# Optimization experiments

Measured on AMD Instinct MI355X. Metric: run time of the kernel, lower is better.

The kernel has to match this reference:

```python
import jax, jax.numpy as jnp
import numpy as np

N_NODES = 100000
N_EDGES = 3200000
DIM = 16


def setup_inputs() -> dict:
    key = jax.random.key(0)
    k1, k2, k3, k4 = jax.random.split(key, 4)
    state_input = jax.random.normal(k1, (N_NODES, DIM), dtype=jnp.float32)
    row = jax.random.randint(k2, (N_EDGES,), 0, N_NODES, dtype=jnp.int32)
    col = jax.random.randint(k3, (N_EDGES,), 0, N_NODES, dtype=jnp.int32)
    edge_weights = jax.random.uniform(k4, (N_EDGES,), dtype=jnp.float32)
    return {"state_input": state_input, "row": row, "col": col,
            "edge_weights": edge_weights}


def reference(state_input, row, col, edge_weights):
    # f_eq: per-dim self dynamics, f(x) = -x  -> [N, dim]
    self_diff = -state_input

    # gather pair endpoints: x_1 = state[col], x_2 = state[row]
    # g_eq: sin(x_2 - x_1) per dim (Kuramoto-style coupling) -> [E, dim]
    neighbor_processed = jnp.sin(state_input[row] - state_input[col])

    # weight by edge weight and scatter-sum into destination nodes (col)
    aggregated_sum = jax.ops.segment_sum(
        neighbor_processed * edge_weights[:, None], col,
        num_segments=state_input.shape[0])  # [N, dim]

    # s_eq: elementwise tanh on aggregated sum
    interact_diff = jnp.tanh(aggregated_sum)

    return (self_diff + interact_diff,
            (state_input, self_diff),
            (aggregated_sum, interact_diff))
```

## Files before the change

kernel.cpp:

```cpp
#include <hip/hip_runtime.h>
#include <hip/hip_fp16.h>
#include <math.h>

#define N_NODES 100000
#define N_EDGES 3200000
#define DIM 16
#define NSZ (N_NODES * DIM)

#define NPB 128
#define NBUCK 782
#define NBLK 512
#define EPB 6256
#define MAXCAP 5120
#define CAP 4864
#define PRK 5

typedef float nvec4 __attribute__((ext_vector_type(4)));

__global__ __launch_bounds__(512)
void prep(const float* __restrict__ state, __half* __restrict__ hs,
          float* __restrict__ out) {
    int i = blockIdx.x * 512 + threadIdx.x;
    if (i >= NSZ / 4) return;
    nvec4 v = __builtin_nontemporal_load(&((const nvec4*)state)[i]);
    union { __half2 h[2]; float2 f; } u;
    u.h[0] = __floats2half2_rn(v.x, v.y);
    u.h[1] = __floats2half2_rn(v.z, v.w);
    ((float2*)hs)[i] = u.f;
    __builtin_nontemporal_store(v, &((nvec4*)(out + 1 * (size_t)NSZ))[i]);
    nvec4 nv = {-v.x, -v.y, -v.z, -v.w};
    __builtin_nontemporal_store(nv, &((nvec4*)(out + 2 * (size_t)NSZ))[i]);
}

#define PACK(c, r, ww) (((unsigned long long)(unsigned)(c) << 47)             \
                      | ((unsigned long long)(unsigned)(r) << 30)             \
                      | (unsigned long long)(__float_as_uint(ww) >> 2))

__global__ __launch_bounds__(512)
void sort_write(const int* __restrict__ row, const int* __restrict__ col,
                const float* __restrict__ w, int* __restrict__ cnt,
                unsigned long long* __restrict__ packed) {
    __shared__ int cur[NBUCK];
    int t = threadIdx.x, blk = blockIdx.x;
    int e0 = blk * EPB;
    int eN = e0 + EPB; if (eN > N_EDGES) eN = N_EDGES;
    int nch = (eN - e0) >> 2;
    const int4*   c4p = (const int4*)(col + e0);
    const int4*   r4p = (const int4*)(row + e0);
    const float4* w4p = (const float4*)(w + e0);

    for (int j = t; j < NBUCK; j += 512) cur[j] = 0;
    __syncthreads();

    unsigned long long pr[16];
    #pragma unroll
    for (int k = 0; k < 4; ++k) {
        int i = t + k * 512;
        if (i < nch) {
            int4 c = c4p[i]; int4 r = r4p[i]; float4 ww = w4p[i];
            pr[4 * k + 0] = PACK(c.x, r.x, ww.x);
            pr[4 * k + 1] = PACK(c.y, r.y, ww.y);
            pr[4 * k + 2] = PACK(c.z, r.z, ww.z);
            pr[4 * k + 3] = PACK(c.w, r.w, ww.w);
            atomicAdd(&cur[c.x >> 7], 1);
            atomicAdd(&cur[c.y >> 7], 1);
            atomicAdd(&cur[c.z >> 7], 1);
            atomicAdd(&cur[c.w >> 7], 1);
        }
    }
    __syncthreads();

    for (int j = t; j < NBUCK; j += 512) {
        int v = cur[j];
        if (v) cur[j] = j * MAXCAP + atomicAdd(&cnt[j], v);
    }
    __syncthreads();

    #pragma unroll
    for (int k = 0; k < 4; ++k) {
        int i = t + k * 512;
        if (i < nch) {
            #pragma unroll
            for (int j = 0; j < 4; ++j) {
                unsigned long long pv = pr[4 * k + j];
                int b = (int)(pv >> 54);
                int pos = atomicAdd(&cur[b], 1);
                packed[pos] = pv;
            }
        }
    }
}

__global__ __launch_bounds__(1024, 8)
void aggregate(const float* __restrict__ state, const __half2* __restrict__ hs2,
               const int* __restrict__ cnt,
               const unsigned long long* __restrict__ packed,
               float* __restrict__ out) {
    __shared__ unsigned long long sbuf[CAP];
    __shared__ int s_cnt[NPB], s_start[NPB], s_cur[NPB];
    __shared__ int s_wsum;
    int nb = blockIdx.x, t = threadIdx.x;
    int q = t & 3, sub = (t >> 2) & 1, g = t >> 3;
    int beg = nb * MAXCAP;
    int end = beg + cnt[nb];
    int n = nb * NPB + g;
    bool valid = (n < N_NODES);
    float4 xx = valid ? ((const float4*)state)[n * 4 + q]
                      : make_float4(0.f, 0.f, 0.f, 0.f);
    float4 acc = {0.f, 0.f, 0.f, 0.f};
    const uint2* hsu = (const uint2*)hs2;

    for (int tbeg = beg; tbeg < end; tbeg += CAP) {
        int tend = tbeg + CAP; if (tend > end) tend = end;
        if (t < NPB) s_cnt[t] = 0;
        __syncthreads();

        unsigned long long pr[PRK];
        #pragma unroll
        for (int k = 0; k < PRK; ++k) {
            int e = tbeg + t + k * 1024;
            if (e < tend) {
                pr[k] = __builtin_nontemporal_load(&packed[e]);
                atomicAdd(&s_cnt[(unsigned)(pr[k] >> 47) & 127u], 1);
            }
        }
        __syncthreads();

        {
            int v = 0, ps = 0;
            if (t < NPB) {
                v = s_cnt[t]; ps = v;
                #pragma unroll
                for (int d = 1; d < 64; d <<= 1) {
                    int u = __shfl_up(ps, d, 64);
                    if ((t & 63) >= d) ps += u;
                }
            }
            if (t == 63) s_wsum = ps;
            __syncthreads();
            if (t < NPB) {
                int ex = ps - v + ((t >= 64) ? s_wsum : 0);
                s_start[t] = ex;
                s_cur[t] = ex;
            }
        }
        __syncthreads();

        #pragma unroll
        for (int k = 0; k < PRK; ++k) {
            int e = tbeg + t + k * 1024;
            if (e < tend) {
                int cl = (int)((pr[k] >> 47) & 127u);
                int pos = atomicAdd(&s_cur[cl], 1);
                sbuf[pos] = pr[k];
            }
        }
        __syncthreads();

        {
            int es = s_start[g], ee = s_cur[g];
            int e = es + sub;
            for (; e + 6 < ee; e += 8) {
                unsigned long long p0 = sbuf[e];
                unsigned long long p1 = sbuf[e + 2];
                unsigned long long p2 = sbuf[e + 4];
                unsigned long long p3 = sbuf[e + 6];
                uint2 h0 = hsu[(unsigned)((p0 >> 30) & 0x1FFFFu) * 4u + q];
                uint2 h1 = hsu[(unsigned)((p1 >> 30) & 0x1FFFFu) * 4u + q];
                uint2 h2 = hsu[(unsigned)((p2 >> 30) & 0x1FFFFu) * 4u + q];
                uint2 h3 = hsu[(unsigned)((p3 >> 30) & 0x1FFFFu) * 4u + q];
                #pragma unroll
                for (int j = 0; j < 4; ++j) {
                    unsigned long long p = (j == 0) ? p0 : (j == 1) ? p1
                                         : (j == 2) ? p2 : p3;
                    uint2 hb = (j == 0) ? h0 : (j == 1) ? h1
                             : (j == 2) ? h2 : h3;
                    float we = __uint_as_float(((unsigned)p & 0x3FFFFFFFu) << 2);
                    float2 lo = __half22float2(*(const __half2*)&hb.x);
                    float2 hi = __half22float2(*(const __half2*)&hb.y);
                    acc.x += __sinf(lo.x - xx.x) * we;
                    acc.y += __sinf(lo.y - xx.y) * we;
                    acc.z += __sinf(hi.x - xx.z) * we;
                    acc.w += __sinf(hi.y - xx.w) * we;
                }
            }
            for (; e < ee; e += 2) {
                unsigned long long p = sbuf[e];
                uint2 hb = hsu[(unsigned)((p >> 30) & 0x1FFFFu) * 4u + q];
                float we = __uint_as_float(((unsigned)p & 0x3FFFFFFFu) << 2);
                float2 lo = __half22float2(*(const __half2*)&hb.x);
                float2 hi = __half22float2(*(const __half2*)&hb.y);
                acc.x += __sinf(lo.x - xx.x) * we;
                acc.y += __sinf(lo.y - xx.y) * we;
                acc.z += __sinf(hi.x - xx.z) * we;
                acc.w += __sinf(hi.y - xx.w) * we;
            }
        }
        __syncthreads();
    }

    acc.x += __shfl_xor(acc.x, 4, 64); acc.y += __shfl_xor(acc.y, 4, 64);
    acc.z += __shfl_xor(acc.z, 4, 64); acc.w += __shfl_xor(acc.w, 4, 64);

    if (valid && sub == 0) {
        float4 th = make_float4(tanhf(acc.x), tanhf(acc.y),
                                tanhf(acc.z), tanhf(acc.w));
        int gdx = n * 4 + q;
        nvec4 v0 = {th.x - xx.x, th.y - xx.y, th.z - xx.z, th.w - xx.w};
        nvec4 v3 = {acc.x, acc.y, acc.z, acc.w};
        nvec4 v4 = {th.x, th.y, th.z, th.w};
        __builtin_nontemporal_store(v0, &((nvec4*)(out + 0 * (size_t)NSZ))[gdx]);
        __builtin_nontemporal_store(v3, &((nvec4*)(out + 3 * (size_t)NSZ))[gdx]);
        __builtin_nontemporal_store(v4, &((nvec4*)(out + 4 * (size_t)NSZ))[gdx]);
    }
}

__global__ __launch_bounds__(256)
void edge_kernel(const float* __restrict__ state, const int* __restrict__ row,
                 const int* __restrict__ col, const float* __restrict__ w,
                 float* __restrict__ agg) {
    int idx = blockIdx.x * blockDim.x + threadIdx.x;
    if (idx >= N_EDGES * 4) return;
    int e = idx >> 2, qq = idx & 3;
    int r = row[e], c = col[e];
    float we = w[e];
    const float4 xr = ((const float4*)state)[r * 4 + qq];
    const float4 xcv = ((const float4*)state)[c * 4 + qq];
    float* dst = agg + c * DIM + qq * 4;
    atomicAdd(dst + 0, sinf(xr.x - xcv.x) * we);
    atomicAdd(dst + 1, sinf(xr.y - xcv.y) * we);
    atomicAdd(dst + 2, sinf(xr.z - xcv.z) * we);
    atomicAdd(dst + 3, sinf(xr.w - xcv.w) * we);
}

__global__ __launch_bounds__(256)
void node_kernel(const float* __restrict__ state, const float* __restrict__ agg,
                 float* __restrict__ out) {
    int idx = blockIdx.x * blockDim.x + threadIdx.x;
    if (idx >= N_NODES * 4) return;
    float4 x = ((const float4*)state)[idx];
    float4 a = ((const float4*)agg)[idx];
    float4 tv = make_float4(tanhf(a.x), tanhf(a.y), tanhf(a.z), tanhf(a.w));
    ((float4*)(out + 0 * NSZ))[idx] = make_float4(tv.x - x.x, tv.y - x.y,
                                                  tv.z - x.z, tv.w - x.w);
    ((float4*)(out + 1 * NSZ))[idx] = x;
    ((float4*)(out + 2 * NSZ))[idx] = make_float4(-x.x, -x.y, -x.z, -x.w);
    ((float4*)(out + 4 * NSZ))[idx] = tv;
}

extern "C" void kernel_launch(void* const* d_in, const int* in_sizes, int n_in,
                              void* d_out, int out_size, void* d_ws, size_t ws_size,
                              hipStream_t stream) {
    const float* state = (const float*)d_in[0];
    const int*   row   = (const int*)d_in[1];
    const int*   col   = (const int*)d_in[2];
    const float* w     = (const float*)d_in[3];
    float* out = (float*)d_out;

    size_t packed_off = 0;
    size_t hs_off     = packed_off + (size_t)NBUCK * MAXCAP * 8;
    size_t cnt_off    = hs_off + (size_t)NSZ * 2;
    size_t needed     = cnt_off + (size_t)NBUCK * 4;

    if (ws_size >= needed) {
        unsigned long long* packed =
            (unsigned long long*)((char*)d_ws + packed_off);
        __half* hs = (__half*)((char*)d_ws + hs_off);
        int* cnt   = (int*)((char*)d_ws + cnt_off);

        (void)hipMemsetAsync(cnt, 0, (size_t)NBUCK * sizeof(int), stream);
        prep<<<(NSZ / 4 + 511) / 512, 512, 0, stream>>>(state, hs, out);
        sort_write<<<NBLK, 512, 0, stream>>>(row, col, w, cnt, packed);
        aggregate<<<NBUCK, 1024, 0, stream>>>(
            state, (const __half2*)hs, cnt, packed, out);
    } else {
        float* agg = out + 3 * NSZ;
        (void)hipMemsetAsync(agg, 0, NSZ * sizeof(float), stream);
        edge_kernel<<<(N_EDGES * 4 + 255) / 256, 256, 0, stream>>>(
            state, row, col, w, agg);
        node_kernel<<<(N_NODES * 4 + 255) / 256, 256, 0, stream>>>(
            state, agg, out);
    }
}
```

Baseline: 162.0 us.

## Replace in-block counting sort with shared-memory atomic accumulation per bucket

The aggregate kernel no longer sub-sorts each bucket's edges by destination node in shared memory (count, scan, scatter, multiple barriers). Instead each thread processes edges in stream order and accumulates sin terms into a shared [128][16] float accumulator with LDS atomics, with node states cached in shared memory. Block size drops from 1024 to 512. This removes the sort passes and their synchronisation but adds four LDS float atomics per edge lane, which may contend when edges share a destination.

```diff
diff --git a/kernel.cpp b/kernel.cpp
--- a/kernel.cpp
+++ b/kernel.cpp
@@ -12,8 +12,6 @@
 #define NBLK 512
 #define EPB 6256
 #define MAXCAP 5120
-#define CAP 4864
-#define PRK 5
 
 typedef float nvec4 __attribute__((ext_vector_type(4)));
 
@@ -91,127 +89,88 @@
     }
 }
 
-__global__ __launch_bounds__(1024, 8)
+__global__ __launch_bounds__(512, 8)
 void aggregate(const float* __restrict__ state, const __half2* __restrict__ hs2,
                const int* __restrict__ cnt,
                const unsigned long long* __restrict__ packed,
                float* __restrict__ out) {
-    __shared__ unsigned long long sbuf[CAP];
-    __shared__ int s_cnt[NPB], s_start[NPB], s_cur[NPB];
-    __shared__ int s_wsum;
+    __shared__ float acc[NPB][DIM];
+    __shared__ float xs[NPB][DIM];
     int nb = blockIdx.x, t = threadIdx.x;
-    int q = t & 3, sub = (t >> 2) & 1, g = t >> 3;
+    int q = t & 3, eg = t >> 2;
+    const uint2* hsu = (const uint2*)hs2;
+
+    {
+        int n0 = nb * NPB;
+        const float* xbase = state + (size_t)n0 * DIM;
+        int lim = (N_NODES - n0) * DIM;
+        if (lim > NPB * DIM) lim = NPB * DIM;
+        for (int i = t; i < NPB * DIM; i += 512) {
+            ((float*)acc)[i] = 0.f;
+            ((float*)xs)[i] = (i < lim) ? xbase[i] : 0.f;
+        }
+    }
+    __syncthreads();
+
     int beg = nb * MAXCAP;
     int end = beg + cnt[nb];
-    int n = nb * NPB + g;
-    bool valid = (n < N_NODES);
-    float4 xx = valid ? ((const float4*)state)[n * 4 + q]
-                      : make_float4(0.f, 0.f, 0.f, 0.f);
-    float4 acc = {0.f, 0.f, 0.f, 0.f};
-    const uint2* hsu = (const uint2*)hs2;
-
-    for (int tbeg = beg; tbeg < end; tbeg += CAP) {
-        int tend = tbeg + CAP; if (tend > end) tend = end;
-        if (t < NPB) s_cnt[t] = 0;
-        __syncthreads();
-
-        unsigned long long pr[PRK];
+    int e = beg + eg;
+    for (; e + 384 < end; e += 512) {
+        unsigned long long p0 = packed[e];
+        unsigned long long p1 = packed[e + 128];
+        unsigned long long p2 = packed[e + 256];
+        unsigned long long p3 = packed[e + 384];
+        uint2 h0 = hsu[(unsigned)((p0 >> 30) & 0x1FFFFu) * 4u + q];
+        uint2 h1 = hsu[(unsigned)((p1 >> 30) & 0x1FFFFu) * 4u + q];
+        uint2 h2 = hsu[(unsigned)((p2 >> 30) & 0x1FFFFu) * 4u + q];
+        uint2 h3 = hsu[(unsigned)((p3 >> 30) & 0x1FFFFu) * 4u + q];
         #pragma unroll
-        for (int k = 0; k < PRK; ++k) {
-            int e = tbeg + t + k * 1024;
-            if (e < tend) {
-                pr[k] = __builtin_nontemporal_load(&packed[e]);
-                atomicAdd(&s_cnt[(unsigned)(pr[k] >> 47) & 127u], 1);
-            }
-        }
-        __syncthreads();
-
-        {
-            int v = 0, ps = 0;
-            if (t < NPB) {
-                v = s_cnt[t]; ps = v;
-                #pragma unroll
-                for (int d = 1; d < 64; d <<= 1) {
-                    int u = __shfl_up(ps, d, 64);
-                    if ((t & 63) >= d) ps += u;
-                }
-            }
-            if (t == 63) s_wsum = ps;
-            __syncthreads();
-            if (t < NPB) {
-                int ex = ps - v + ((t >= 64) ? s_wsum : 0);
-                s_start[t] = ex;
-                s_cur[t] = ex;
-            }
-        }
-        __syncthreads();
-
-        #pragma unroll
-        for (int k = 0; k < PRK; ++k) {
-            int e = tbeg + t + k * 1024;
-            if (e < tend) {
-                int cl = (int)((pr[k] >> 47) & 127u);
-                int pos = atomicAdd(&s_cur[cl], 1);
-                sbuf[pos] = pr[k];
-            }
-        }
-        __syncthreads();
-
-        {
-            int es = s_start[g], ee = s_cur[g];
-            int e = es + sub;
-            for (; e + 6 < ee; e += 8) {
-                unsigned long long p0 = sbuf[e];
-                unsigned long long p1 = sbuf[e + 2];
-                unsigned long long p2 = sbuf[e + 4];
-                unsigned long long p3 = sbuf[e + 6];
-                uint2 h0 = hsu[(unsigned)((p0 >> 30) & 0x1FFFFu) * 4u + q];
-                uint2 h1 = hsu[(unsigned)((p1 >> 30) & 0x1FFFFu) * 4u + q];
-                uint2 h2 = hsu[(unsigned)((p2 >> 30) & 0x1FFFFu) * 4u + q];
-                uint2 h3 = hsu[(unsigned)((p3 >> 30) & 0x1FFFFu) * 4u + q];
-                #pragma unroll
-                for (int j = 0; j < 4; ++j) {
-                    unsigned long long p = (j == 0) ? p0 : (j == 1) ? p1
-                                         : (j == 2) ? p2 : p3;
-                    uint2 hb = (j == 0) ? h0 : (j == 1) ? h1
-                             : (j == 2) ? h2 : h3;
-                    float we = __uint_as_float(((unsigned)p & 0x3FFFFFFFu) << 2);
-                    float2 lo = __half22float2(*(const __half2*)&hb.x);
-                    float2 hi = __half22float2(*(const __half2*)&hb.y);
-                    acc.x += __sinf(lo.x - xx.x) * we;
-                    acc.y += __sinf(lo.y - xx.y) * we;
-                    acc.z += __sinf(hi.x - xx.z) * we;
-                    acc.w += __sinf(hi.y - xx.w) * we;
-                }
-            }
-            for (; e < ee; e += 2) {
-                unsigned long long p = sbuf[e];
-                uint2 hb = hsu[(unsigned)((p >> 30) & 0x1FFFFu) * 4u + q];
-                float we = __uint_as_float(((unsigned)p & 0x3FFFFFFFu) << 2);
-                float2 lo = __half22float2(*(const __half2*)&hb.x);
-                float2 hi = __half22float2(*(const __half2*)&hb.y);
-                acc.x += __sinf(lo.x - xx.x) * we;
-                acc.y += __sinf(lo.y - xx.y) * we;
-                acc.z += __sinf(hi.x - xx.z) * we;
-                acc.w += __sinf(hi.y - xx.w) * we;
-            }
-        }
-        __syncthreads();
-    }
-
-    acc.x += __shfl_xor(acc.x, 4, 64); acc.y += __shfl_xor(acc.y, 4, 64);
-    acc.z += __shfl_xor(acc.z, 4, 64); acc.w += __shfl_xor(acc.w, 4, 64);
-
-    if (valid && sub == 0) {
-        float4 th = make_float4(tanhf(acc.x), tanhf(acc.y),
-                                tanhf(acc.z), tanhf(acc.w));
-        int gdx = n * 4 + q;
-        nvec4 v0 = {th.x - xx.x, th.y - xx.y, th.z - xx.z, th.w - xx.w};
-        nvec4 v3 = {acc.x, acc.y, acc.z, acc.w};
-        nvec4 v4 = {th.x, th.y, th.z, th.w};
-        __builtin_nontemporal_store(v0, &((nvec4*)(out + 0 * (size_t)NSZ))[gdx]);
-        __builtin_nontemporal_store(v3, &((nvec4*)(out + 3 * (size_t)NSZ))[gdx]);
-        __builtin_nontemporal_store(v4, &((nvec4*)(out + 4 * (size_t)NSZ))[gdx]);
+        for (int j = 0; j < 4; ++j) {
+            unsigned long long p = (j == 0) ? p0 : (j == 1) ? p1
+                                 : (j == 2) ? p2 : p3;
+            uint2 hb = (j == 0) ? h0 : (j == 1) ? h1 : (j == 2) ? h2 : h3;
+            int cl = (int)((p >> 47) & 127u);
+            float we = __uint_as_float(((unsigned)p & 0x3FFFFFFFu) << 2);
+            float2 lo = __half22float2(*(const __half2*)&hb.x);
+            float2 hi = __half22float2(*(const __half2*)&hb.y);
+            float4 xc = *(const float4*)&xs[cl][q * 4];
+            atomicAdd(&acc[cl][q * 4 + 0], __sinf(lo.x - xc.x) * we);
+            atomicAdd(&acc[cl][q * 4 + 1], __sinf(lo.y - xc.y) * we);
+            atomicAdd(&acc[cl][q * 4 + 2], __sinf(hi.x - xc.z) * we);
+            atomicAdd(&acc[cl][q * 4 + 3], __sinf(hi.y - xc.w) * we);
+        }
+    }
+    for (; e < end; e += 128) {
+        unsigned long long p = packed[e];
+        uint2 hb = hsu[(unsigned)((p >> 30) & 0x1FFFFu) * 4u + q];
+        int cl = (int)((p >> 47) & 127u);
+        float we = __uint_as_float(((unsigned)p & 0x3FFFFFFFu) << 2);
+        float2 lo = __half22float2(*(const __half2*)&hb.x);
+        float2 hi = __half22float2(*(const __half2*)&hb.y);
+        float4 xc = *(const float4*)&xs[cl][q * 4];
+        atomicAdd(&acc[cl][q * 4 + 0], __sinf(lo.x - xc.x) * we);
+        atomicAdd(&acc[cl][q * 4 + 1], __sinf(lo.y - xc.y) * we);
+        atomicAdd(&acc[cl][q * 4 + 2], __sinf(hi.x - xc.z) * we);
+        atomicAdd(&acc[cl][q * 4 + 3], __sinf(hi.y - xc.w) * we);
+    }
+    __syncthreads();
+
+    {
+        int s = t >> 2;
+        int n = nb * NPB + s;
+        if (n < N_NODES) {
+            float4 a  = *(const float4*)&acc[s][q * 4];
+            float4 xxv = *(const float4*)&xs[s][q * 4];
+            float4 th = make_float4(tanhf(a.x), tanhf(a.y),
+                                    tanhf(a.z), tanhf(a.w));
+            int gdx = n * 4 + q;
+            nvec4 v0 = {th.x - xxv.x, th.y - xxv.y, th.z - xxv.z, th.w - xxv.w};
+            nvec4 v3 = {a.x, a.y, a.z, a.w};
+            nvec4 v4 = {th.x, th.y, th.z, th.w};
+            __builtin_nontemporal_store(v0, &((nvec4*)(out + 0 * (size_t)NSZ))[gdx]);
+            __builtin_nontemporal_store(v3, &((nvec4*)(out + 3 * (size_t)NSZ))[gdx]);
+            __builtin_nontemporal_store(v4, &((nvec4*)(out + 4 * (size_t)NSZ))[gdx]);
+        }
     }
 }
 
@@ -271,7 +230,7 @@
         (void)hipMemsetAsync(cnt, 0, (size_t)NBUCK * sizeof(int), stream);
         prep<<<(NSZ / 4 + 511) / 512, 512, 0, stream>>>(state, hs, out);
         sort_write<<<NBLK, 512, 0, stream>>>(row, col, w, cnt, packed);
-        aggregate<<<NBUCK, 1024, 0, stream>>>(
+        aggregate<<<NBUCK, 512, 0, stream>>>(
             state, (const __half2*)hs, cnt, packed, out);
     } else {
         float* agg = out + 3 * NSZ;
```

Result: slower. 471.1 us (+190.7%).
